# Kernel optimization log

Hardware: AMD Instinct MI355X
Metric: run time of the kernel (lower is better)

Reference implementation:

```python
import jax, jax.numpy as jnp
import numpy as np


def setup_inputs() -> dict:
    key = jax.random.key(0)
    k1, k2 = jax.random.split(key)
    x = jax.random.normal(k1, (8, 2048, 1024), dtype=jnp.float32)
    kernel = jax.random.normal(k2, (3, 1024, 1024), dtype=jnp.float32) * 0.02
    return {"x": x, "kernel": kernel}


def reference(x, kernel):
    # x: [b, s, d]; kernel: [3, d, o]
    q = jnp.einsum('bsd,do->bso', x, kernel[0])
    k = jnp.einsum('bsd,do->bso', x, kernel[1])
    v = jnp.einsum('bsd,do->bso', x, kernel[2])
    seq_len = x.shape[1]
    # NOTE: original scales by sqrt(seq_len), not sqrt(d_k)
    scores = jnp.einsum('bqo,bko->bqk', q, k) / (seq_len ** 0.5)
    attn = jax.nn.softmax(scores, axis=-1)
    return jnp.einsum('bqk,bko->bqo', attn, v)
```

## Files before the change

kernel.cpp:

```cpp
#include <hip/hip_runtime.h>
#include <stdint.h>

typedef __bf16  bf16x8  __attribute__((ext_vector_type(8)));
typedef float   f32x4   __attribute__((ext_vector_type(4)));
typedef unsigned short ushort8 __attribute__((ext_vector_type(8)));
typedef unsigned short ushort4v __attribute__((ext_vector_type(4)));

#define DEV __device__ __forceinline__

DEV unsigned short f2bf(float f) {
    union { float f; unsigned u; } v; v.f = f;
    unsigned u = v.u;
    return (unsigned short)((u + 0x7FFFu + ((u >> 16) & 1u)) >> 16);
}
DEV float bf2f(unsigned short h) {
    union { unsigned u; float f; } v; v.u = ((unsigned)h) << 16;
    return v.f;
}

DEV void gload16(const void* g, void* l) {
    __builtin_amdgcn_global_load_lds(
        (const __attribute__((address_space(1))) unsigned int*)g,
        (__attribute__((address_space(3))) unsigned int*)l, 16, 0, 0);
}

template<bool OUT_BF16>
__global__ __launch_bounds__(512, 2)
void gemm256(const unsigned short* __restrict__ A, long lda, long sA,
             const unsigned short* __restrict__ B, long ldb, long sB,
             void* __restrict__ Cv, long ldc, long sC,
             int N, int K, float alpha)
{
    __shared__ __attribute__((aligned(16))) char sm[131072];

    const int bz = blockIdx.z;
    A += (long)bz * sA;
    B += (long)bz * sB;

    const int tiles_n = N >> 8;
    int bid = blockIdx.x;
    const int nwg = gridDim.x;
    {
        const int q = nwg >> 3, r = nwg & 7;
        const int xcd = bid & 7, idx = bid >> 3;
        bid = (xcd < r ? xcd * (q + 1) : r * (q + 1) + (xcd - r) * q) + idx;
    }
    const long brow = (long)(bid / tiles_n) << 8;
    const long bcol = (long)(bid % tiles_n) << 8;

    const int t = threadIdx.x;
    const int w = t >> 6, lane = t & 63;
    const int wr = w >> 2, wc = w & 3;
    const int lr = lane & 15, lk = lane >> 4;

    const int srow = (w << 3) + (lane >> 3);
    const int scol = ((lane & 7) ^ (lane >> 3)) << 3;
    const unsigned short* gA = A + (brow + srow) * lda + scol;
    const unsigned short* gB = B + (bcol + srow) * ldb + scol;
    char* const dstA = sm + w * 1024;
    char* const dstB = sm + 32768 + w * 1024;
    const long lda64 = 64 * lda, ldaH = 128 * lda;
    const long ldb64 = 64 * ldb, ldbH = 128 * ldb;

    const int rsw0 = ((lk ^ (lr & 7)) << 4);
    const int aoff = wr * 16384 + lr * 128;
    const int boff = 32768 + (wc >> 1) * 16384 + (((wc & 1) << 6) + lr) * 128;

    f32x4 acc[8][4];
#pragma unroll
    for (int m = 0; m < 8; ++m)
#pragma unroll
        for (int n = 0; n < 4; ++n) acc[m][n] = 0.f;

    const int nk = K >> 6;

    gload16(gA,                dstA);
    gload16(gA + lda64,        dstA + 8192);
    gload16(gA + ldaH,         dstA + 16384);
    gload16(gA + ldaH + lda64, dstA + 16384 + 8192);
    gload16(gB,                dstB);
    gload16(gB + ldb64,        dstB + 8192);
    gload16(gB + ldbH,         dstB + 16384);
    gload16(gB + ldbH + ldb64, dstB + 16384 + 8192);
    if (nk > 1) {
        gload16(gA + 64,                dstA + 65536);
        gload16(gA + 64 + lda64,        dstA + 65536 + 8192);
        gload16(gA + 64 + ldaH,         dstA + 65536 + 16384);
        gload16(gA + 64 + ldaH + lda64, dstA + 65536 + 16384 + 8192);
        asm volatile("s_waitcnt vmcnt(4)" ::: "memory");
    } else {
        asm volatile("s_waitcnt vmcnt(0)" ::: "memory");
    }
    __builtin_amdgcn_s_barrier();

    const unsigned short* gAk = gA;
    const unsigned short* gBk = gB;

    for (int kt = 0; kt < nk; ++kt) {
        const int buf = kt & 1;
        const char* sa = sm + buf * 65536 + aoff;
        const char* sb = sm + buf * 65536 + boff;
        char* const dA = dstA + buf * 65536;
        char* const dB = dstB + (buf ^ 1) * 65536;
        bf16x8 a0[4][2], a1[4][2], b01[2][2], b23[2][2];

#pragma unroll
        for (int m = 0; m < 4; ++m) {
            a0[m][0] = *(const bf16x8*)(sa + m * 2048 + rsw0);
            a0[m][1] = *(const bf16x8*)(sa + m * 2048 + (rsw0 ^ 64));
        }
#pragma unroll
        for (int n = 0; n < 2; ++n) {
            b01[n][0] = *(const bf16x8*)(sb + n * 2048 + rsw0);
            b01[n][1] = *(const bf16x8*)(sb + n * 2048 + (rsw0 ^ 64));
        }
        if (kt + 1 < nk) {
            gload16(gBk + 64,         dB);
            gload16(gBk + 64 + ldb64, dB + 8192);
        }
        __builtin_amdgcn_s_barrier();
        __builtin_amdgcn_s_setprio(1);
#pragma unroll
        for (int ks = 0; ks < 2; ++ks)
#pragma unroll
            for (int m = 0; m < 4; ++m)
#pragma unroll
                for (int n = 0; n < 2; ++n)
                    acc[m][n] = __builtin_amdgcn_mfma_f32_16x16x32_bf16(
                        a0[m][ks], b01[n][ks], acc[m][n], 0, 0, 0);
        __builtin_amdgcn_s_setprio(0);
        __builtin_amdgcn_s_barrier();

#pragma unroll
        for (int n = 0; n < 2; ++n) {
            b23[n][0] = *(const bf16x8*)(sb + (n + 2) * 2048 + rsw0);
            b23[n][1] = *(const bf16x8*)(sb + (n + 2) * 2048 + (rsw0 ^ 64));
        }
        if (kt + 1 < nk) {
            gload16(gBk + 64 + ldbH,         dB + 16384);
            gload16(gBk + 64 + ldbH + ldb64, dB + 16384 + 8192);
        }
        __builtin_amdgcn_s_barrier();
        __builtin_amdgcn_s_setprio(1);
#pragma unroll
        for (int ks = 0; ks < 2; ++ks)
#pragma unroll
            for (int m = 0; m < 4; ++m)
#pragma unroll
                for (int n = 0; n < 2; ++n)
                    acc[m][n + 2] = __builtin_amdgcn_mfma_f32_16x16x32_bf16(
                        a0[m][ks], b23[n][ks], acc[m][n + 2], 0, 0, 0);
        __builtin_amdgcn_s_setprio(0);
        __builtin_amdgcn_s_barrier();

#pragma unroll
        for (int m = 0; m < 4; ++m) {
            a1[m][0] = *(const bf16x8*)(sa + (m + 4) * 2048 + rsw0);
            a1[m][1] = *(const bf16x8*)(sa + (m + 4) * 2048 + (rsw0 ^ 64));
        }
        if (kt + 2 < nk) {
            gload16(gAk + 128,         dA);
            gload16(gAk + 128 + lda64, dA + 8192);
        }
        __builtin_amdgcn_s_barrier();
        __builtin_amdgcn_s_setprio(1);
#pragma unroll
        for (int ks = 0; ks < 2; ++ks)
#pragma unroll
            for (int m = 0; m < 4; ++m)
#pragma unroll
                for (int n = 0; n < 2; ++n)
                    acc[m + 4][n] = __builtin_amdgcn_mfma_f32_16x16x32_bf16(
                        a1[m][ks], b01[n][ks], acc[m + 4][n], 0, 0, 0);
        __builtin_amdgcn_s_setprio(0);
        __builtin_amdgcn_s_barrier();

        if (kt + 2 < nk) {
            gload16(gAk + 128 + ldaH,         dA + 16384);
            gload16(gAk + 128 + ldaH + lda64, dA + 16384 + 8192);
        }
        __builtin_amdgcn_s_setprio(1);
#pragma unroll
        for (int ks = 0; ks < 2; ++ks)
#pragma unroll
            for (int m = 0; m < 4; ++m)
#pragma unroll
                for (int n = 0; n < 2; ++n)
                    acc[m + 4][n + 2] = __builtin_amdgcn_mfma_f32_16x16x32_bf16(
                        a1[m][ks], b23[n][ks], acc[m + 4][n + 2], 0, 0, 0);
        __builtin_amdgcn_s_setprio(0);
        if (kt + 2 < nk) {
            asm volatile("s_waitcnt vmcnt(4)" ::: "memory");
        } else if (kt + 1 < nk) {
            asm volatile("s_waitcnt vmcnt(0)" ::: "memory");
        }
        __builtin_amdgcn_s_barrier();

        gAk += 64; gBk += 64;
    }

    const long r0 = brow + wr * 128;
    const long c0 = bcol + wc * 64;
    if (OUT_BF16) {
        unsigned short* C = (unsigned short*)Cv + (long)bz * sC;
#pragma unroll
        for (int m = 0; m < 8; ++m)
#pragma unroll
            for (int n = 0; n < 4; ++n) {
                const long c = c0 + n * 16 + lr;
#pragma unroll
                for (int j = 0; j < 4; ++j) {
                    const long r = r0 + m * 16 + lk * 4 + j;
                    C[r * ldc + c] = f2bf(acc[m][n][j] * alpha);
                }
            }
    } else {
        float* C = (float*)Cv + (long)bz * sC;
#pragma unroll
        for (int m = 0; m < 8; ++m)
#pragma unroll
            for (int n = 0; n < 4; ++n) {
                const long c = c0 + n * 16 + lr;
#pragma unroll
                for (int j = 0; j < 4; ++j) {
                    const long r = r0 + m * 16 + lk * 4 + j;
                    C[r * ldc + c] = acc[m][n][j] * alpha;
                }
            }
    }
}

__global__ __launch_bounds__(256)
void conv_x(const f32x4* __restrict__ X, ushort4v* __restrict__ Y, long n4)
{
    long i = (long)blockIdx.x * 256 + threadIdx.x;
    const long stride = (long)gridDim.x * 256;
    for (; i < n4; i += stride) {
        f32x4 v = X[i];
        ushort4v o;
#pragma unroll
        for (int j = 0; j < 4; ++j) o[j] = f2bf(v[j]);
        Y[i] = o;
    }
}

__global__ __launch_bounds__(256)
void conv_w(const float* __restrict__ W, unsigned short* __restrict__ Wt)
{
    __shared__ unsigned short tile[64][65];
    const long hofs = (long)blockIdx.z * 1048576;
    const int d0 = blockIdx.x * 64;
    const int o0 = blockIdx.y * 64;
    const int t = threadIdx.x;
    const int c  = t & 63;
    const int r0 = t >> 6;
#pragma unroll
    for (int rr = 0; rr < 64; rr += 4) {
        const int r = rr + r0;
        tile[r][c] = f2bf(W[hofs + (long)(d0 + r) * 1024 + (o0 + c)]);
    }
    __syncthreads();
#pragma unroll
    for (int rr = 0; rr < 64; rr += 4) {
        const int r = rr + r0;
        Wt[hofs + (long)(o0 + r) * 1024 + (d0 + c)] = tile[c][r];
    }
}

__global__ __launch_bounds__(256)
void softmax_rows(unsigned short* __restrict__ P)
{
    __shared__ float red[4];
    const int t = threadIdx.x;
    const int lane = t & 63, wave = t >> 6;

    for (int r = 0; r < 8; ++r) {
        unsigned short* p = P + ((long)blockIdx.x * 8 + r) * 2048;
        ushort8 u = *(const ushort8*)(p + t * 8);
        float x[8];
        float mx = -3.0e38f;
#pragma unroll
        for (int j = 0; j < 8; ++j) { x[j] = bf2f(u[j]); mx = fmaxf(mx, x[j]); }
#pragma unroll
        for (int o = 1; o < 64; o <<= 1) mx = fmaxf(mx, __shfl_xor(mx, o));
        if (lane == 0) red[wave] = mx;
        __syncthreads();
        mx = fmaxf(fmaxf(red[0], red[1]), fmaxf(red[2], red[3]));
        __syncthreads();

        float e[8], s = 0.f;
#pragma unroll
        for (int j = 0; j < 8; ++j) { e[j] = __expf(x[j] - mx); s += e[j]; }
#pragma unroll
        for (int o = 1; o < 64; o <<= 1) s += __shfl_xor(s, o);
        if (lane == 0) red[wave] = s;
        __syncthreads();
        s = red[0] + red[1] + red[2] + red[3];
        __syncthreads();

        const float inv = 1.0f / s;
        ushort8 o8;
#pragma unroll
        for (int j = 0; j < 8; ++j) o8[j] = f2bf(e[j] * inv);
        *(ushort8*)(p + t * 8) = o8;
    }
}

extern "C" void kernel_launch(void* const* d_in, const int* in_sizes, int n_in,
                              void* d_out, int out_size, void* d_ws, size_t ws_size,
                              hipStream_t stream)
{
    const float* x = (const float*)d_in[0];
    const float* w = (const float*)d_in[1];
    float* out = (float*)d_out;

    const long BS = 16384;
    const long D  = 1024;
    const long S  = 2048;

    char* ws = (char*)d_ws;
    unsigned short* Xb = (unsigned short*)ws; ws += BS * D * 2;
    unsigned short* Wt = (unsigned short*)ws; ws += 3L * D * D * 2;
    unsigned short* QK = (unsigned short*)ws; ws += BS * 2 * D * 2;
    unsigned short* Vt = (unsigned short*)ws; ws += D * BS * 2;
    unsigned short* P  = (unsigned short*)ws; ws += 8L * S * S * 2;

    conv_x<<<4096, 256, 0, stream>>>((const f32x4*)x, (ushort4v*)Xb, BS * D / 4);
    conv_w<<<dim3(16, 16, 3), 256, 0, stream>>>(w, Wt);

    gemm256<true><<<dim3((BS / 256) * (2048 / 256), 1, 1), 512, 0, stream>>>(
        Xb, D, 0, Wt, D, 0, QK, 2 * D, 0, 2048, (int)D, 1.f);

    gemm256<true><<<dim3((1024 / 256) * (BS / 256), 1, 1), 512, 0, stream>>>(
        Wt + 2L * D * D, D, 0, Xb, D, 0, Vt, BS, 0, (int)BS, (int)D, 1.f);

    gemm256<true><<<dim3((S / 256) * (S / 256), 1, 8), 512, 0, stream>>>(
        QK, 2 * D, S * 2 * D,
        QK + D, 2 * D, S * 2 * D,
        P, S, S * S,
        (int)S, (int)D, 0.022097086912079612f);

    softmax_rows<<<2048, 256, 0, stream>>>(P);

    gemm256<false><<<dim3((S / 256) * (1024 / 256), 1, 8), 512, 0, stream>>>(
        P, S, S * S,
        Vt, BS, S,
        out, D, S * D,
        1024, (int)S, 1.f);
}
```

Baseline: 389.6 us.

## Software-pipeline LDS fragment reads one phase ahead of MFMA in bf16 GEMM

Restructures the GEMM main loop so each phase's LDS fragment reads for the next MFMA group are issued before the current MFMA group runs, including prefetching the next k-tile's a0/b01 fragments from the other buffer. The prologue now loads both A and B for the first two k-tiles, and B's next-next tile is fetched in one batch. The number of barriers per iteration drops from eight to four, with explicit lgkmcnt waits and sched_barriers fencing each phase. The aim is to hide LDS latency behind MFMA and cut barrier stalls, at the cost of more live registers and a prologue that assumes at least two k-tiles.

```diff
diff --git a/kernel.cpp b/kernel.cpp
--- a/kernel.cpp
+++ b/kernel.cpp
@@ -82,28 +82,22 @@
     gload16(gB + ldb64,        dstB + 8192);
     gload16(gB + ldbH,         dstB + 16384);
     gload16(gB + ldbH + ldb64, dstB + 16384 + 8192);
-    if (nk > 1) {
-        gload16(gA + 64,                dstA + 65536);
-        gload16(gA + 64 + lda64,        dstA + 65536 + 8192);
-        gload16(gA + 64 + ldaH,         dstA + 65536 + 16384);
-        gload16(gA + 64 + ldaH + lda64, dstA + 65536 + 16384 + 8192);
-        asm volatile("s_waitcnt vmcnt(4)" ::: "memory");
-    } else {
-        asm volatile("s_waitcnt vmcnt(0)" ::: "memory");
-    }
+    gload16(gA + 64,                dstA + 65536);
+    gload16(gA + 64 + lda64,        dstA + 65536 + 8192);
+    gload16(gA + 64 + ldaH,         dstA + 65536 + 16384);
+    gload16(gA + 64 + ldaH + lda64, dstA + 65536 + 16384 + 8192);
+    gload16(gB + 64,                dstB + 65536);
+    gload16(gB + 64 + ldb64,        dstB + 65536 + 8192);
+    gload16(gB + 64 + ldbH,         dstB + 65536 + 16384);
+    gload16(gB + 64 + ldbH + ldb64, dstB + 65536 + 16384 + 8192);
+    asm volatile("s_waitcnt vmcnt(8)" ::: "memory");
     __builtin_amdgcn_s_barrier();
 
-    const unsigned short* gAk = gA;
-    const unsigned short* gBk = gB;
-
-    for (int kt = 0; kt < nk; ++kt) {
-        const int buf = kt & 1;
-        const char* sa = sm + buf * 65536 + aoff;
-        const char* sb = sm + buf * 65536 + boff;
-        char* const dA = dstA + buf * 65536;
-        char* const dB = dstB + (buf ^ 1) * 65536;
-        bf16x8 a0[4][2], a1[4][2], b01[2][2], b23[2][2];
-
+    bf16x8 a0[4][2], a1[4][2], b01[2][2], b23[2][2];
+
+    {
+        const char* sa = sm + aoff;
+        const char* sb = sm + boff;
 #pragma unroll
         for (int m = 0; m < 4; ++m) {
             a0[m][0] = *(const bf16x8*)(sa + m * 2048 + rsw0);
@@ -114,11 +108,25 @@
             b01[n][0] = *(const bf16x8*)(sb + n * 2048 + rsw0);
             b01[n][1] = *(const bf16x8*)(sb + n * 2048 + (rsw0 ^ 64));
         }
-        if (kt + 1 < nk) {
-            gload16(gBk + 64,         dB);
-            gload16(gBk + 64 + ldb64, dB + 8192);
-        }
-        __builtin_amdgcn_s_barrier();
+    }
+
+    const unsigned short* gAk = gA;
+    const unsigned short* gBk = gB;
+
+    for (int kt = 0; kt < nk; ++kt) {
+        const int p = kt & 1;
+        const char* sa  = sm + p * 65536 + aoff;
+        const char* sb  = sm + p * 65536 + boff;
+        const char* saq = sm + (p ^ 1) * 65536 + aoff;
+        const char* sbq = sm + (p ^ 1) * 65536 + boff;
+        char* const dA  = dstA + p * 65536;
+        char* const dB  = dstB + p * 65536;
+
+#pragma unroll
+        for (int n = 0; n < 2; ++n) {
+            b23[n][0] = *(const bf16x8*)(sb + (n + 2) * 2048 + rsw0);
+            b23[n][1] = *(const bf16x8*)(sb + (n + 2) * 2048 + (rsw0 ^ 64));
+        }
         __builtin_amdgcn_s_setprio(1);
 #pragma unroll
         for (int ks = 0; ks < 2; ++ks)
@@ -129,18 +137,21 @@
                     acc[m][n] = __builtin_amdgcn_mfma_f32_16x16x32_bf16(
                         a0[m][ks], b01[n][ks], acc[m][n], 0, 0, 0);
         __builtin_amdgcn_s_setprio(0);
+        asm volatile("s_waitcnt lgkmcnt(0)" ::: "memory");
+        __builtin_amdgcn_sched_barrier(0);
         __builtin_amdgcn_s_barrier();
 
 #pragma unroll
-        for (int n = 0; n < 2; ++n) {
-            b23[n][0] = *(const bf16x8*)(sb + (n + 2) * 2048 + rsw0);
-            b23[n][1] = *(const bf16x8*)(sb + (n + 2) * 2048 + (rsw0 ^ 64));
-        }
-        if (kt + 1 < nk) {
-            gload16(gBk + 64 + ldbH,         dB + 16384);
-            gload16(gBk + 64 + ldbH + ldb64, dB + 16384 + 8192);
-        }
-        __builtin_amdgcn_s_barrier();
+        for (int m = 0; m < 4; ++m) {
+            a1[m][0] = *(const bf16x8*)(sa + (m + 4) * 2048 + rsw0);
+            a1[m][1] = *(const bf16x8*)(sa + (m + 4) * 2048 + (rsw0 ^ 64));
+        }
+        if (kt + 2 < nk) {
+            gload16(gBk + 128,                dB);
+            gload16(gBk + 128 + ldb64,        dB + 8192);
+            gload16(gBk + 128 + ldbH,         dB + 16384);
+            gload16(gBk + 128 + ldbH + ldb64, dB + 16384 + 8192);
+        }
         __builtin_amdgcn_s_setprio(1);
 #pragma unroll
         for (int ks = 0; ks < 2; ++ks)
@@ -151,18 +162,27 @@
                     acc[m][n + 2] = __builtin_amdgcn_mfma_f32_16x16x32_bf16(
                         a0[m][ks], b23[n][ks], acc[m][n + 2], 0, 0, 0);
         __builtin_amdgcn_s_setprio(0);
+        if (kt + 2 < nk) {
+            asm volatile("s_waitcnt vmcnt(4) lgkmcnt(0)" ::: "memory");
+        } else if (kt + 1 < nk) {
+            asm volatile("s_waitcnt vmcnt(0) lgkmcnt(0)" ::: "memory");
+        } else {
+            asm volatile("s_waitcnt lgkmcnt(0)" ::: "memory");
+        }
+        __builtin_amdgcn_sched_barrier(0);
         __builtin_amdgcn_s_barrier();
 
-#pragma unroll
-        for (int m = 0; m < 4; ++m) {
-            a1[m][0] = *(const bf16x8*)(sa + (m + 4) * 2048 + rsw0);
-            a1[m][1] = *(const bf16x8*)(sa + (m + 4) * 2048 + (rsw0 ^ 64));
+        if (kt + 1 < nk) {
+#pragma unroll
+            for (int m = 0; m < 4; ++m) {
+                a0[m][0] = *(const bf16x8*)(saq + m * 2048 + rsw0);
+                a0[m][1] = *(const bf16x8*)(saq + m * 2048 + (rsw0 ^ 64));
+            }
         }
         if (kt + 2 < nk) {
             gload16(gAk + 128,         dA);
             gload16(gAk + 128 + lda64, dA + 8192);
         }
-        __builtin_amdgcn_s_barrier();
         __builtin_amdgcn_s_setprio(1);
 #pragma unroll
         for (int ks = 0; ks < 2; ++ks)
@@ -173,8 +193,17 @@
                     acc[m + 4][n] = __builtin_amdgcn_mfma_f32_16x16x32_bf16(
                         a1[m][ks], b01[n][ks], acc[m + 4][n], 0, 0, 0);
         __builtin_amdgcn_s_setprio(0);
+        asm volatile("s_waitcnt lgkmcnt(0)" ::: "memory");
+        __builtin_amdgcn_sched_barrier(0);
         __builtin_amdgcn_s_barrier();
 
+        if (kt + 1 < nk) {
+#pragma unroll
+            for (int n = 0; n < 2; ++n) {
+                b01[n][0] = *(const bf16x8*)(sbq + n * 2048 + rsw0);
+                b01[n][1] = *(const bf16x8*)(sbq + n * 2048 + (rsw0 ^ 64));
+            }
+        }
         if (kt + 2 < nk) {
             gload16(gAk + 128 + ldaH,         dA + 16384);
             gload16(gAk + 128 + ldaH + lda64, dA + 16384 + 8192);
@@ -189,11 +218,8 @@
                     acc[m + 4][n + 2] = __builtin_amdgcn_mfma_f32_16x16x32_bf16(
                         a1[m][ks], b23[n][ks], acc[m + 4][n + 2], 0, 0, 0);
         __builtin_amdgcn_s_setprio(0);
-        if (kt + 2 < nk) {
-            asm volatile("s_waitcnt vmcnt(4)" ::: "memory");
-        } else if (kt + 1 < nk) {
-            asm volatile("s_waitcnt vmcnt(0)" ::: "memory");
-        }
+        asm volatile("s_waitcnt lgkmcnt(0)" ::: "memory");
+        __builtin_amdgcn_sched_barrier(0);
         __builtin_amdgcn_s_barrier();
 
         gAk += 64; gBk += 64;
```

Measured after the change: 472.9 us. 21.4% more time.
